# Performance work log

Hardware: AMD Instinct MI355X
Metric: run time of the kernel (lower is better)

The kernel has to match this reference:

```python
import jax, jax.numpy as jnp
import numpy as np

N = 6000
E = 48000
NODE_TYPE_SIZE = 9
OBSTACLE = 1
RADIUS = 0.03
EPS = 1e-8


def _safe_norm(x):
    # L2 norm over last dim, safe gradient at 0 (diagonal / self edges)
    sq = jnp.sum(x * x, axis=-1, keepdims=True)
    return jnp.where(sq > 0, jnp.sqrt(jnp.where(sq > 0, sq, 1.0)), 0.0)


def setup_inputs() -> dict:
    key = jax.random.key(0)
    ks = jax.random.split(key, 12)
    world_pos = jax.random.uniform(ks[0], (N, 3), dtype=jnp.float32)
    prev_world_pos = world_pos + 0.001 * jax.random.normal(ks[1], (N, 3), dtype=jnp.float32)
    mesh_pos = jax.random.uniform(ks[2], (N, 2), dtype=jnp.float32)
    node_type = jax.random.randint(ks[3], (N, 1), 0, NODE_TYPE_SIZE)
    senders = jax.random.randint(ks[4], (E,), 0, N)
    receivers = jax.random.randint(ks[5], (E,), 0, N)
    node_mean = jax.random.normal(ks[6], (3 + NODE_TYPE_SIZE,), dtype=jnp.float32)
    node_std = 0.5 + jax.random.uniform(ks[7], (3 + NODE_TYPE_SIZE,), dtype=jnp.float32)
    mesh_mean = jax.random.normal(ks[8], (7,), dtype=jnp.float32)
    mesh_std = 0.5 + jax.random.uniform(ks[9], (7,), dtype=jnp.float32)
    world_mean = jax.random.normal(ks[10], (4,), dtype=jnp.float32)
    world_std = 0.5 + jax.random.uniform(ks[11], (4,), dtype=jnp.float32)
    return dict(world_pos=world_pos, prev_world_pos=prev_world_pos, mesh_pos=mesh_pos,
                node_type=node_type, senders=senders, receivers=receivers,
                node_mean=node_mean, node_std=node_std, mesh_mean=mesh_mean,
                mesh_std=mesh_std, world_mean=world_mean, world_std=world_std)


def reference(world_pos, prev_world_pos, mesh_pos, node_type, senders, receivers,
              node_mean, node_std, mesh_mean, mesh_std, world_mean, world_std):
    n = world_pos.shape[0]
    # --- node features: velocity + one-hot node type, normalized ---
    velocity = world_pos - prev_world_pos
    one_hot = jax.nn.one_hot(node_type[:, 0], NODE_TYPE_SIZE, dtype=world_pos.dtype)
    node_feat = jnp.concatenate([velocity, one_hot], axis=-1)  # [N, 12]
    node_out = (node_feat - node_mean) / jnp.maximum(node_std, EPS)
    # --- radius graph: dense squared-distance matrix + threshold (cdist < r) ---
    sq = jnp.sum(world_pos * world_pos, axis=-1)
    d2 = sq[:, None] + sq[None, :] - 2.0 * (world_pos @ world_pos.T)  # [N, N]
    conn = d2 < RADIUS ** 2
    conn = conn & ~jnp.eye(n, dtype=bool)              # fill_diagonal_(False)
    conn = conn.at[senders, receivers].set(False)      # drop existing mesh edges
    obstacle = node_type[:, 0] == OBSTACLE
    conn = conn & ~obstacle[None, :]                   # no edges into obstacle nodes
    # --- world edge features (dense, masked by connectivity) ---
    rel_world = world_pos[None, :, :] - world_pos[:, None, :]  # [i,j] = pos[j]-pos[i]
    world_feat = jnp.concatenate([rel_world, _safe_norm(rel_world)], axis=-1)  # [N, N, 4]
    world_out = (world_feat - world_mean) / jnp.maximum(world_std, EPS)
    world_out = jnp.where(conn[:, :, None], world_out, 0.0)
    # --- mesh edge features: gather on edge list, normalize ---
    rw = world_pos[senders] - world_pos[receivers]     # [E, 3]
    rm = mesh_pos[senders] - mesh_pos[receivers]       # [E, 2]
    mesh_feat = jnp.concatenate([rw, _safe_norm(rw), rm, _safe_norm(rm)], axis=-1)  # [E, 7]
    mesh_out = (mesh_feat - mesh_mean) / jnp.maximum(mesh_std, EPS)
    # --- unsorted_segment_operation: scatter_add mesh edge features to receivers ---
    agg = jax.ops.segment_sum(mesh_out, receivers, num_segments=n)  # [N, 7]
    return node_out, mesh_out, world_out, agg
```

## Files before the change

kernel.cpp:

```cpp
#include <hip/hip_runtime.h>

#define N_NODES 6000
#define N_EDGES 48000
#define NODE_TYPE_SIZE 9
#define OBSTACLE 1
#define RADIUS2 0.0009f
#define EPS_F 1e-8f

#define OFF_NODE  0
#define OFF_MESH  72000
#define OFF_WORLD 408000
#define OFF_AGG   144408000

#define AUX_NODE_END 72000
#define AUX_AGG_END  (72000 + 42000)
#define AUX_TBL_END  (72000 + 42000 + 6000)

#define JPT 8

typedef float floatx4 __attribute__((ext_vector_type(4)));

__global__ void k_aux(const float* __restrict__ wp, const float* __restrict__ pwp,
                      const int* __restrict__ nt, const float* __restrict__ nmean,
                      const float* __restrict__ nstd, float* __restrict__ node_out,
                      float* __restrict__ agg, float4* __restrict__ tbl) {
    int t = blockIdx.x * blockDim.x + threadIdx.x;
    if (t < AUX_NODE_END) {
        int n = t / 12;
        int f = t - n * 12;
        float feat;
        if (f < 3) feat = wp[n * 3 + f] - pwp[n * 3 + f];
        else       feat = (nt[n] == f - 3) ? 1.0f : 0.0f;
        node_out[t] = (feat - nmean[f]) / fmaxf(nstd[f], EPS_F);
    } else if (t < AUX_AGG_END) {
        agg[t - AUX_NODE_END] = 0.0f;
    } else if (t < AUX_TBL_END) {
        int j = t - AUX_AGG_END;
        float x = wp[3 * j + 0], y = wp[3 * j + 1], z = wp[3 * j + 2];
        float sq = x * x + y * y + z * z;
        if (nt[j] == OBSTACLE) sq = 1e30f;
        tbl[j] = make_float4(x, y, z, sq);
    }
}

__global__ void k_mesh(const float* __restrict__ wp, const float* __restrict__ mp,
                       const int* __restrict__ senders, const int* __restrict__ receivers,
                       const float* __restrict__ mean, const float* __restrict__ stdv,
                       float* __restrict__ mesh_out, float* __restrict__ agg) {
    int e = blockIdx.x * blockDim.x + threadIdx.x;
    if (e >= N_EDGES) return;
    int s = senders[e];
    int r = receivers[e];
    float rwx = wp[3 * s + 0] - wp[3 * r + 0];
    float rwy = wp[3 * s + 1] - wp[3 * r + 1];
    float rwz = wp[3 * s + 2] - wp[3 * r + 2];
    float nrw = sqrtf(rwx * rwx + rwy * rwy + rwz * rwz);
    float rmx = mp[2 * s + 0] - mp[2 * r + 0];
    float rmy = mp[2 * s + 1] - mp[2 * r + 1];
    float nrm = sqrtf(rmx * rmx + rmy * rmy);
    float feats[7] = {rwx, rwy, rwz, nrw, rmx, rmy, nrm};
    #pragma unroll
    for (int k = 0; k < 7; ++k) {
        float o = (feats[k] - mean[k]) / fmaxf(stdv[k], EPS_F);
        mesh_out[e * 7 + k] = o;
        atomicAdd(&agg[r * 7 + k], o);
    }
}

__global__ void k_world(const float4* __restrict__ tbl, const float* __restrict__ mean,
                        const float* __restrict__ stdv, floatx4* __restrict__ world_out) {
    const int i = blockIdx.y;
    const int j_base = blockIdx.x * (256 * JPT) + threadIdx.x;
    const float4 pi = tbl[i];
    const float sqi = pi.x * pi.x + pi.y * pi.y + pi.z * pi.z;
    const float m0 = mean[0], m1 = mean[1], m2 = mean[2], m3 = mean[3];
    const float s0 = fmaxf(stdv[0], EPS_F), s1 = fmaxf(stdv[1], EPS_F);
    const float s2 = fmaxf(stdv[2], EPS_F), s3 = fmaxf(stdv[3], EPS_F);
    floatx4* __restrict__ row = world_out + (size_t)i * N_NODES;
    #pragma unroll
    for (int k = 0; k < JPT; ++k) {
        int j = j_base + k * 256;
        if (j < N_NODES) {
            float4 pj = tbl[j];
            float dot = pi.x * pj.x + pi.y * pj.y + pi.z * pj.z;
            float d2 = sqi + pj.w - 2.0f * dot;
            floatx4 v = (floatx4){0.0f, 0.0f, 0.0f, 0.0f};
            if (d2 < RADIUS2 && i != j) {
                float rx = pj.x - pi.x, ry = pj.y - pi.y, rz = pj.z - pi.z;
                float nrm = sqrtf(rx * rx + ry * ry + rz * rz);
                v.x = (rx  - m0) / s0;
                v.y = (ry  - m1) / s1;
                v.z = (rz  - m2) / s2;
                v.w = (nrm - m3) / s3;
            }
            __builtin_nontemporal_store(v, &row[j]);
        }
    }
}

__global__ void k_edge_zero(const int* __restrict__ senders, const int* __restrict__ receivers,
                            float4* __restrict__ world_out) {
    int e = blockIdx.x * blockDim.x + threadIdx.x;
    if (e >= N_EDGES) return;
    world_out[(size_t)senders[e] * N_NODES + receivers[e]] = make_float4(0.0f, 0.0f, 0.0f, 0.0f);
}

extern "C" void kernel_launch(void* const* d_in, const int* in_sizes, int n_in,
                              void* d_out, int out_size, void* d_ws, size_t ws_size,
                              hipStream_t stream) {
    const float* wp    = (const float*)d_in[0];
    const float* pwp   = (const float*)d_in[1];
    const float* mp    = (const float*)d_in[2];
    const int*   nt    = (const int*)d_in[3];
    const int*   snd   = (const int*)d_in[4];
    const int*   rcv   = (const int*)d_in[5];
    const float* nmean = (const float*)d_in[6];
    const float* nstd  = (const float*)d_in[7];
    const float* mmean = (const float*)d_in[8];
    const float* mstd  = (const float*)d_in[9];
    const float* wmean = (const float*)d_in[10];
    const float* wstd  = (const float*)d_in[11];

    float* out       = (float*)d_out;
    float* node_out  = out + OFF_NODE;
    float* mesh_out  = out + OFF_MESH;
    float* world_out = out + OFF_WORLD;
    float* agg       = out + OFF_AGG;
    float4* tbl      = (float4*)d_ws;

    k_aux<<<(AUX_TBL_END + 255) / 256, 256, 0, stream>>>(
        wp, pwp, nt, nmean, nstd, node_out, agg, tbl);

    k_mesh<<<(N_EDGES + 255) / 256, 256, 0, stream>>>(
        wp, mp, snd, rcv, mmean, mstd, mesh_out, agg);

    dim3 wgrid((N_NODES + 256 * JPT - 1) / (256 * JPT), N_NODES);
    k_world<<<wgrid, 256, 0, stream>>>(tbl, wmean, wstd, (floatx4*)world_out);

    k_edge_zero<<<(N_EDGES + 255) / 256, 256, 0, stream>>>(snd, rcv, (float4*)world_out);
}
```

Measured before the change: 141.8 us.

## Replace dense world-edge writer with memset plus sparse tiled pair kernel

Zeroes the dense world-edge output with a memset, then runs a tiled pair kernel that caches a block of sender positions in shared memory and writes only the pairs within the radius. Receivers that are obstacle nodes are skipped early. The aim is to use the memset's fast fill path and avoid computing and writing zero vectors element by element. This adds a separate memset pass and scattered non-coalesced writes for the pairs that are connected.

Result: slower. 168.7 us (+18.9%).

```diff
diff --git a/kernel.cpp b/kernel.cpp
--- a/kernel.cpp
+++ b/kernel.cpp
@@ -16,9 +16,7 @@
 #define AUX_AGG_END  (72000 + 42000)
 #define AUX_TBL_END  (72000 + 42000 + 6000)
 
-#define JPT 8
-
-typedef float floatx4 __attribute__((ext_vector_type(4)));
+#define TI 128
 
 __global__ void k_aux(const float* __restrict__ wp, const float* __restrict__ pwp,
                       const int* __restrict__ nt, const float* __restrict__ nmean,
@@ -67,33 +65,38 @@
     }
 }
 
-__global__ void k_world(const float4* __restrict__ tbl, const float* __restrict__ mean,
-                        const float* __restrict__ stdv, floatx4* __restrict__ world_out) {
-    const int i = blockIdx.y;
-    const int j_base = blockIdx.x * (256 * JPT) + threadIdx.x;
-    const float4 pi = tbl[i];
-    const float sqi = pi.x * pi.x + pi.y * pi.y + pi.z * pi.z;
+__global__ void k_pairs(const float4* __restrict__ tbl, const float* __restrict__ mean,
+                        const float* __restrict__ stdv, float4* __restrict__ world_out) {
+    __shared__ float4 si[TI];
+    const int i0 = blockIdx.y * TI;
+    const int ni = (N_NODES - i0 < TI) ? (N_NODES - i0) : TI;
+    if (threadIdx.x < ni) si[threadIdx.x] = tbl[i0 + threadIdx.x];
+    __syncthreads();
+
+    const int j = blockIdx.x * 256 + threadIdx.x;
+    if (j >= N_NODES) return;
+    const float4 pj = tbl[j];
+    if (pj.w > 1e29f) return;
+
     const float m0 = mean[0], m1 = mean[1], m2 = mean[2], m3 = mean[3];
     const float s0 = fmaxf(stdv[0], EPS_F), s1 = fmaxf(stdv[1], EPS_F);
     const float s2 = fmaxf(stdv[2], EPS_F), s3 = fmaxf(stdv[3], EPS_F);
-    floatx4* __restrict__ row = world_out + (size_t)i * N_NODES;
-    #pragma unroll
-    for (int k = 0; k < JPT; ++k) {
-        int j = j_base + k * 256;
-        if (j < N_NODES) {
-            float4 pj = tbl[j];
-            float dot = pi.x * pj.x + pi.y * pj.y + pi.z * pj.z;
-            float d2 = sqi + pj.w - 2.0f * dot;
-            floatx4 v = (floatx4){0.0f, 0.0f, 0.0f, 0.0f};
-            if (d2 < RADIUS2 && i != j) {
-                float rx = pj.x - pi.x, ry = pj.y - pi.y, rz = pj.z - pi.z;
-                float nrm = sqrtf(rx * rx + ry * ry + rz * rz);
-                v.x = (rx  - m0) / s0;
-                v.y = (ry  - m1) / s1;
-                v.z = (rz  - m2) / s2;
-                v.w = (nrm - m3) / s3;
-            }
-            __builtin_nontemporal_store(v, &row[j]);
+
+    for (int k = 0; k < ni; ++k) {
+        float4 pi = si[k];
+        float sqi = pi.x * pi.x + pi.y * pi.y + pi.z * pi.z;
+        float dot = pi.x * pj.x + pi.y * pj.y + pi.z * pj.z;
+        float d2 = sqi + pj.w - 2.0f * dot;
+        int i = i0 + k;
+        if (d2 < RADIUS2 && i != j) {
+            float rx = pj.x - pi.x, ry = pj.y - pi.y, rz = pj.z - pi.z;
+            float nrm = sqrtf(rx * rx + ry * ry + rz * rz);
+            float4 v;
+            v.x = (rx  - m0) / s0;
+            v.y = (ry  - m1) / s1;
+            v.z = (rz  - m2) / s2;
+            v.w = (nrm - m3) / s3;
+            world_out[(size_t)i * N_NODES + j] = v;
         }
     }
 }
@@ -134,8 +137,10 @@
     k_mesh<<<(N_EDGES + 255) / 256, 256, 0, stream>>>(
         wp, mp, snd, rcv, mmean, mstd, mesh_out, agg);
 
-    dim3 wgrid((N_NODES + 256 * JPT - 1) / (256 * JPT), N_NODES);
-    k_world<<<wgrid, 256, 0, stream>>>(tbl, wmean, wstd, (floatx4*)world_out);
+    hipMemsetAsync(world_out, 0, (size_t)N_NODES * N_NODES * 4 * sizeof(float), stream);
+
+    dim3 pgrid((N_NODES + 255) / 256, (N_NODES + TI - 1) / TI);
+    k_pairs<<<pgrid, 256, 0, stream>>>(tbl, wmean, wstd, (float4*)world_out);
 
     k_edge_zero<<<(N_EDGES + 255) / 256, 256, 0, stream>>>(snd, rcv, (float4*)world_out);
 }
```
